# Optimization experiments

Measured on AMD Instinct MI355X. Metric: run time of the kernel, lower is better.

Reference implementation:

```python
import jax, jax.numpy as jnp
import numpy as np

CAM_FL = 540.0
CAM_W, CAM_H = 640, 480
FILTER_STD = 1.0
FILTER_SCALE = 1.0
RADIUS = int(np.ceil(2.0 * FILTER_STD))  # truncate Gaussian footprint at 2 std
K = 2 * RADIUS + 1                        # 5x5 footprint


def setup_inputs() -> dict:
    key = jax.random.key(0)
    k1, k2, k3, k4 = jax.random.split(key, 4)
    B, N = 4, 200000
    locs = jax.random.normal(k1, (B, N, 3), jnp.float32) * 2.0
    camera_pose = jax.random.normal(k2, (B, 3), jnp.float32) * 0.1
    camera_rot = jax.random.normal(k3, (B, 4), jnp.float32)
    # depth in [0, 10): some particles occluded, some visible
    depth_mask = jax.random.uniform(k4, (B, CAM_H, CAM_W), jnp.float32) * 10.0
    return {"locs": locs, "camera_pose": camera_pose,
            "camera_rot": camera_rot, "depth_mask": depth_mask}


def _rot_from_quat(q):
    # Matches torch _rotationMatrixFromQuaternion layout: R[b, i, j]
    qx, qy, qz, qw = q[:, 0], q[:, 1], q[:, 2], q[:, 3]
    qx2, qy2, qz2 = qx * qx, qy * qy, qz * qz
    qxqy, qxqz, qxqw = qx * qy, qx * qz, qx * qw
    qyqz, qyqw, qzqw = qy * qz, qy * qw, qz * qw
    r00 = 1 - 2 * qy2 - 2 * qz2
    r10 = 2 * qxqy - 2 * qzqw
    r20 = 2 * qxqz + 2 * qyqw
    r01 = 2 * qxqy + 2 * qzqw
    r11 = 1 - 2 * qx2 - 2 * qz2
    r21 = 2 * qyqz - 2 * qxqw
    r02 = 2 * qxqz - 2 * qyqw
    r12 = 2 * qyqz + 2 * qxqw
    r22 = 1 - 2 * qx2 - 2 * qy2
    row0 = jnp.stack([r00, r01, r02], axis=-1)
    row1 = jnp.stack([r10, r11, r12], axis=-1)
    row2 = jnp.stack([r20, r21, r22], axis=-1)
    return jnp.stack([row0, row1, row2], axis=-2)  # (B,3,3)


def reference(locs, camera_pose, camera_rot, depth_mask):
    B, N, _ = locs.shape
    # transform into camera frame
    p = locs - camera_pose[:, None, :]
    q = camera_rot / jnp.sqrt(jnp.sum(camera_rot ** 2, axis=1, keepdims=True))
    q = q * jnp.array([-1.0, -1.0, -1.0, 1.0], q.dtype)  # conjugate -> inverse rotation
    R = jax.lax.stop_gradient(_rot_from_quat(q))          # torch uses quat.data (detached)
    p = jnp.einsum('bni,bij->bnj', p, R)                  # torch.bmm(locs, rot)
    x, y, z = p[..., 0], p[..., 1], p[..., 2]
    zsafe = jnp.where(z > 0, z, 1.0)
    # pinhole projection, principal point at image center
    px = x / zsafe * CAM_FL + CAM_W / 2.0   # (B,N)
    py = y / zsafe * CAM_FL + CAM_H / 2.0
    offs = jnp.arange(K, dtype=jnp.int32) - RADIUS
    jx = jnp.floor(px).astype(jnp.int32)[..., None] + offs   # (B,N,K) column idx
    iy = jnp.floor(py).astype(jnp.int32)[..., None] + offs   # (B,N,K) row idx
    dx = jx.astype(px.dtype) - px[..., None]
    dy = iy.astype(py.dtype) - py[..., None]
    # (B,N,K,K) Gaussian footprint weights
    w = FILTER_SCALE * jnp.exp(-(dy[..., :, None] ** 2 + dx[..., None, :] ** 2)
                               / (2.0 * FILTER_STD ** 2))
    ii = jnp.broadcast_to(iy[..., :, None], w.shape)
    jj = jnp.broadcast_to(jx[..., None, :], w.shape)
    inb = (ii >= 0) & (ii < CAM_H) & (jj >= 0) & (jj < CAM_W)
    iic = jnp.clip(ii, 0, CAM_H - 1)
    jjc = jnp.clip(jj, 0, CAM_W - 1)
    bidx = jnp.arange(B, dtype=jnp.int32)[:, None, None, None]
    d = depth_mask[bidx, iic, jjc]          # per-pixel occlusion depth
    zb = z[..., None, None]
    valid = inb & (zb > 0) & (zb <= d)      # in front of camera and not occluded
    w = jnp.where(valid, w, 0.0)
    out = jnp.zeros((B, CAM_H, CAM_W), locs.dtype)
    out = out.at[bidx, iic, jjc].add(w)
    return out
```

## Files before the change

### kernel.cpp

```cpp
#include <hip/hip_runtime.h>

#define CAM_FL 540.0f
#define CAM_W  640
#define CAM_H  480
#define RADIUS 2
#define KSIZE  (2 * RADIUS + 1)
#define TAPS   (KSIZE * KSIZE)
#define BLK    256
#define TILE   16
#define TX_N   (CAM_W / TILE)
#define TY_N   (CAM_H / TILE)
#define TILES_PER_B (TX_N * TY_N)
#define REC_OFF 65536


__global__ __launch_bounds__(BLK) void project_bin_kernel(
    const float* __restrict__ locs,
    const float* __restrict__ camera_pose,
    const float* __restrict__ camera_rot,
    const float* __restrict__ depth,
    float* __restrict__ out,
    int* __restrict__ tileCnt,
    float4* __restrict__ tileRec,
    int N, int CAP)
{
#pragma clang fp contract(off)
    const int b = blockIdx.y;
    const int n = blockIdx.x * blockDim.x + threadIdx.x;
    if (n >= N) return;

    const float qx_raw = camera_rot[b * 4 + 0];
    const float qy_raw = camera_rot[b * 4 + 1];
    const float qz_raw = camera_rot[b * 4 + 2];
    const float qw_raw = camera_rot[b * 4 + 3];
    const float norm2 = ((qx_raw * qx_raw + qy_raw * qy_raw) + qz_raw * qz_raw) + qw_raw * qw_raw;
    const float s = sqrtf(norm2);
    const float qx = -(qx_raw / s);
    const float qy = -(qy_raw / s);
    const float qz = -(qz_raw / s);
    const float qw =  (qw_raw / s);

    const float qx2 = qx * qx, qy2 = qy * qy, qz2 = qz * qz;
    const float qxqy = qx * qy, qxqz = qx * qz, qxqw = qx * qw;
    const float qyqz = qy * qz, qyqw = qy * qw, qzqw = qz * qw;
    const float r00 = (1.0f - 2.0f * qy2) - 2.0f * qz2;
    const float r10 = 2.0f * qxqy - 2.0f * qzqw;
    const float r20 = 2.0f * qxqz + 2.0f * qyqw;
    const float r01 = 2.0f * qxqy + 2.0f * qzqw;
    const float r11 = (1.0f - 2.0f * qx2) - 2.0f * qz2;
    const float r21 = 2.0f * qyqz - 2.0f * qxqw;
    const float r02 = 2.0f * qxqz - 2.0f * qyqw;
    const float r12 = 2.0f * qyqz + 2.0f * qxqw;
    const float r22 = (1.0f - 2.0f * qx2) - 2.0f * qy2;

    const float cpx = camera_pose[b * 3 + 0];
    const float cpy = camera_pose[b * 3 + 1];
    const float cpz = camera_pose[b * 3 + 2];

    const float p0 = locs[(size_t)(b * N + n) * 3 + 0] - cpx;
    const float p1 = locs[(size_t)(b * N + n) * 3 + 1] - cpy;
    const float p2 = locs[(size_t)(b * N + n) * 3 + 2] - cpz;

    const float x = (p0 * r00 + p1 * r10) + p2 * r20;
    const float y = (p0 * r01 + p1 * r11) + p2 * r21;
    const float z = (p0 * r02 + p1 * r12) + p2 * r22;

    if (!(z > 0.0f)) return;

    const float px = (x / z) * CAM_FL + (float)CAM_W * 0.5f;
    const float py = (y / z) * CAM_FL + (float)CAM_H * 0.5f;

    if (!(px >= -(float)RADIUS && px < (float)(CAM_W + RADIUS) &&
          py >= -(float)RADIUS && py < (float)(CAM_H + RADIUS)))
        return;

    const int iy0 = (int)floorf(py);
    const int jx0 = (int)floorf(px);

    const int tyLo = max(0, iy0 - RADIUS) / TILE;
    const int tyHi = min(CAM_H - 1, iy0 + RADIUS) / TILE;
    const int txLo = max(0, jx0 - RADIUS) / TILE;
    const int txHi = min(CAM_W - 1, jx0 + RADIUS) / TILE;

    for (int ty = tyLo; ty <= tyHi; ++ty) {
        for (int tx = txLo; tx <= txHi; ++tx) {
            const int tileId = b * TILES_PER_B + ty * TX_N + tx;
            const int idx = atomicAdd(&tileCnt[tileId], 1);
            if (idx < CAP) {
                tileRec[(size_t)tileId * CAP + idx] = make_float4(px, py, z, 0.0f);
            } else {
                for (int t = 0; t < TAPS; ++t) {
                    const int ti = t / KSIZE, tj = t - (t / KSIZE) * KSIZE;
                    const int iy = iy0 + ti - RADIUS;
                    const int jx = jx0 + tj - RADIUS;
                    if ((iy >> 4) == ty && (jx >> 4) == tx) {
                        const size_t pix = (size_t)b * (CAM_H * CAM_W) + (size_t)iy * CAM_W + jx;
                        const float d = depth[pix];
                        if (z <= d) {
                            const float dyf = (float)iy - py;
                            const float dxf = (float)jx - px;
                            atomicAdd(&out[pix], __expf(-(dyf * dyf + dxf * dxf) * 0.5f));
                        }
                    }
                }
            }
        }
    }
}

__global__ __launch_bounds__(BLK) void tile_gather_kernel(
    const float* __restrict__ depth,
    float* __restrict__ out,
    const int* __restrict__ tileCnt,
    const float4* __restrict__ tileRec,
    int CAP)
{
#pragma clang fp contract(off)
    __shared__ float4 sRec[BLK];

    const int tileId = blockIdx.x;
    const int b  = tileId / TILES_PER_B;
    const int r  = tileId - b * TILES_PER_B;
    const int ty = r / TX_N;
    const int tx = r - ty * TX_N;

    const int tid = threadIdx.x;
    const int iy  = ty * TILE + (tid >> 4);
    const int jx  = tx * TILE + (tid & 15);

    const size_t pix = (size_t)b * (CAM_H * CAM_W) + (size_t)iy * CAM_W + jx;
    const float d    = depth[pix];
    const float prev = out[pix];

    const int cnt = min(tileCnt[tileId], CAP);
    float acc = 0.0f;

    for (int base = 0; base < cnt; base += BLK) {
        const int m = min(BLK, cnt - base);
        if (tid < m)
            sRec[tid] = tileRec[(size_t)tileId * CAP + base + tid];
        __syncthreads();

        for (int s = 0; s < m; ++s) {
            const float4 rec = sRec[s];
            const int riy0 = (int)floorf(rec.y);
            const int rjx0 = (int)floorf(rec.x);
            const int di = iy - riy0;
            const int dj = jx - rjx0;
            if (di >= -RADIUS && di <= RADIUS && dj >= -RADIUS && dj <= RADIUS &&
                rec.z <= d) {
                const float dyf = (float)iy - rec.y;
                const float dxf = (float)jx - rec.x;
                acc += __expf(-(dyf * dyf + dxf * dxf) * 0.5f);
            }
        }
        __syncthreads();
    }

    out[pix] = prev + acc;
}

extern "C" void kernel_launch(void* const* d_in, const int* in_sizes, int n_in,
                              void* d_out, int out_size, void* d_ws, size_t ws_size,
                              hipStream_t stream) {
    const float* locs        = (const float*)d_in[0];
    const float* camera_pose = (const float*)d_in[1];
    const float* camera_rot  = (const float*)d_in[2];
    const float* depth_mask  = (const float*)d_in[3];
    float* out = (float*)d_out;

    const int B = in_sizes[1] / 3;
    const int N = in_sizes[0] / (3 * B);
    const int chunks = (N + BLK - 1) / BLK;
    const int nTiles = B * TILES_PER_B;

    int*    tileCnt = (int*)d_ws;
    float4* tileRec = (float4*)((char*)d_ws + REC_OFF);
    long long capLL = ((long long)ws_size - REC_OFF) / ((long long)nTiles * 16);
    int CAP = (int)(capLL < 0 ? 0 : (capLL > 4096 ? 4096 : capLL));

    (void)hipMemsetAsync(d_out, 0, (size_t)out_size * sizeof(float), stream);
    (void)hipMemsetAsync(d_ws, 0, (size_t)nTiles * sizeof(int), stream);

    dim3 block(BLK, 1, 1);
    project_bin_kernel<<<dim3(chunks, B, 1), block, 0, stream>>>(
        locs, camera_pose, camera_rot, depth_mask, out, tileCnt, tileRec, N, CAP);
    tile_gather_kernel<<<dim3(nTiles, 1, 1), block, 0, stream>>>(
        depth_mask, out, tileCnt, tileRec, CAP);
}
```

Baseline: 99.07 us.

## Switch tile pass from per-pixel gather to per-tap scatter into shared memory

The tile kernel stops having every pixel thread test every record in the tile and instead spreads the record×tap pairs across threads. Each valid tap adds its Gaussian weight into a shared-memory accumulator with an LDS atomic. This cuts the work per record from 256 pixel checks to 25 taps, in exchange for shared atomics, integer division per tap, and a summation order that can change float results.

```diff
diff --git a/kernel.cpp b/kernel.cpp
--- a/kernel.cpp
+++ b/kernel.cpp
@@ -108,7 +108,7 @@
     }
 }
 
-__global__ __launch_bounds__(BLK) void tile_gather_kernel(
+__global__ __launch_bounds__(BLK) void tile_accum_kernel(
     const float* __restrict__ depth,
     float* __restrict__ out,
     const int* __restrict__ tileCnt,
@@ -116,6 +116,8 @@
     int CAP)
 {
 #pragma clang fp contract(off)
+    __shared__ float  sAcc[BLK];
+    __shared__ float  sDepth[BLK];
     __shared__ float4 sRec[BLK];
 
     const int tileId = blockIdx.x;
@@ -123,41 +125,52 @@
     const int r  = tileId - b * TILES_PER_B;
     const int ty = r / TX_N;
     const int tx = r - ty * TX_N;
+    const int tyBase = ty * TILE;
+    const int txBase = tx * TILE;
 
     const int tid = threadIdx.x;
-    const int iy  = ty * TILE + (tid >> 4);
-    const int jx  = tx * TILE + (tid & 15);
-
+    const int iy  = tyBase + (tid >> 4);
+    const int jx  = txBase + (tid & 15);
     const size_t pix = (size_t)b * (CAM_H * CAM_W) + (size_t)iy * CAM_W + jx;
-    const float d    = depth[pix];
-    const float prev = out[pix];
+
+    sDepth[tid] = depth[pix];
+    sAcc[tid]   = 0.0f;
 
     const int cnt = min(tileCnt[tileId], CAP);
-    float acc = 0.0f;
+    const float4* recs = tileRec + (size_t)tileId * CAP;
 
     for (int base = 0; base < cnt; base += BLK) {
         const int m = min(BLK, cnt - base);
-        if (tid < m)
-            sRec[tid] = tileRec[(size_t)tileId * CAP + base + tid];
         __syncthreads();
-
-        for (int s = 0; s < m; ++s) {
-            const float4 rec = sRec[s];
-            const int riy0 = (int)floorf(rec.y);
-            const int rjx0 = (int)floorf(rec.x);
-            const int di = iy - riy0;
-            const int dj = jx - rjx0;
-            if (di >= -RADIUS && di <= RADIUS && dj >= -RADIUS && dj <= RADIUS &&
-                rec.z <= d) {
-                const float dyf = (float)iy - rec.y;
-                const float dxf = (float)jx - rec.x;
-                acc += __expf(-(dyf * dyf + dxf * dxf) * 0.5f);
+        if (tid < m) sRec[tid] = recs[base + tid];
+        __syncthreads();
+
+        const int total = m * TAPS;
+        for (int t = tid; t < total; t += BLK) {
+            const int si  = t / TAPS;
+            const int tap = t - si * TAPS;
+            const int ti  = tap / KSIZE;
+            const int tj  = tap - ti * KSIZE;
+
+            const float4 rec = sRec[si];
+            const int riy = (int)floorf(rec.y) + ti - RADIUS;
+            const int rjx = (int)floorf(rec.x) + tj - RADIUS;
+            const int liy = riy - tyBase;
+            const int ljx = rjx - txBase;
+            if ((unsigned)liy < TILE && (unsigned)ljx < TILE) {
+                const int lpix = (liy << 4) + ljx;
+                if (rec.z <= sDepth[lpix]) {
+                    const float dyf = (float)riy - rec.y;
+                    const float dxf = (float)rjx - rec.x;
+                    const float w = __expf(-(dyf * dyf + dxf * dxf) * 0.5f);
+                    atomicAdd(&sAcc[lpix], w);
+                }
             }
         }
-        __syncthreads();
     }
 
-    out[pix] = prev + acc;
+    __syncthreads();
+    out[pix] = out[pix] + sAcc[tid];
 }
 
 extern "C" void kernel_launch(void* const* d_in, const int* in_sizes, int n_in,
@@ -185,6 +198,6 @@
     dim3 block(BLK, 1, 1);
     project_bin_kernel<<<dim3(chunks, B, 1), block, 0, stream>>>(
         locs, camera_pose, camera_rot, depth_mask, out, tileCnt, tileRec, N, CAP);
-    tile_gather_kernel<<<dim3(nTiles, 1, 1), block, 0, stream>>>(
+    tile_accum_kernel<<<dim3(nTiles, 1, 1), block, 0, stream>>>(
         depth_mask, out, tileCnt, tileRec, CAP);
 }
```

Result: no change. 97.27 us (-1.8%).
